# Kernel tuning notes

Measured on AMD Instinct MI355X. Metric: run time of the kernel, lower is better.

The kernel has to match this reference:

```python
import math
import jax, jax.numpy as jnp
import numpy as np

WH, WW = 8, 8
NUM_HEADS = 4
EMBED_DIMS = 128
N_TOK = WH * WW

# --- static relative position index (N, N) ---
_coords = np.stack(np.meshgrid(np.arange(WH), np.arange(WW), indexing='ij')).reshape(2, -1)
_rel = (_coords[:, :, None] - _coords[:, None, :]).transpose(1, 2, 0).copy()
_rel[..., 0] += WH - 1
_rel[..., 1] += WW - 1
_rel[..., 0] *= 2 * WW - 1
REL_INDEX = _rel.sum(-1)  # (N, N) ints in [0, (2Wh-1)(2Ww-1))

# --- static log-spaced relative coords table ((2Wh-1)*(2Ww-1), 2) ---
_ch = np.arange(-(WH - 1), WH, dtype=np.float32)
_cw = np.arange(-(WW - 1), WW, dtype=np.float32)
_tab = np.stack(np.meshgrid(_ch, _cw, indexing='ij')).reshape(2, -1).T.copy()
_tab[:, 0] /= WH - 1
_tab[:, 1] /= WW - 1
_tab *= 8
COORDS_TABLE = np.sign(_tab) * np.log2(np.abs(_tab) + 1.0) / math.log2(8)  # (225, 2)


def setup_inputs() -> dict:
    key = jax.random.key(0)
    ks = jax.random.split(key, 8)
    B_ = 8192
    C = EMBED_DIMS
    H = NUM_HEADS
    return {
        'x': jax.random.normal(ks[0], (B_, N_TOK, C), dtype=jnp.float32),
        'mask': jnp.zeros((256, N_TOK, N_TOK), dtype=jnp.float32),
        'qkv_w': jax.random.normal(ks[1], (3 * C, C), dtype=jnp.float32) * 0.02,
        'q_bias': jnp.zeros((C,), dtype=jnp.float32),
        'v_bias': jnp.zeros((C,), dtype=jnp.float32),
        'logit_scale': jnp.full((H, 1, 1), math.log(10.0), dtype=jnp.float32),
        'cpb_w1': jax.random.normal(ks[2], (512, 2), dtype=jnp.float32) * 0.02,
        'cpb_b1': jnp.zeros((512,), dtype=jnp.float32),
        'cpb_w2': jax.random.normal(ks[3], (H, 512), dtype=jnp.float32) * 0.02,
        'proj_w': jax.random.normal(ks[4], (C, C), dtype=jnp.float32) * 0.02,
        'proj_b': jnp.zeros((C,), dtype=jnp.float32),
    }


def reference(x, mask, qkv_w, q_bias, v_bias, logit_scale, cpb_w1, cpb_b1, cpb_w2, proj_w, proj_b):
    B_, N, C = x.shape
    H = NUM_HEADS
    D = C // H
    # qkv with q/v bias only (k bias is zero)
    qkv_b = jnp.concatenate([q_bias, jnp.zeros_like(v_bias), v_bias])
    qkv = x @ qkv_w.T + qkv_b                           # (B_, N, 3C)
    qkv = qkv.reshape(B_, N, 3, H, D).transpose(2, 0, 3, 1, 4)
    q, k, v = qkv[0], qkv[1], qkv[2]                    # (B_, H, N, D)
    # cosine attention
    qn = q / jnp.clip(jnp.linalg.norm(q, axis=-1, keepdims=True), 1e-12)
    kn = k / jnp.clip(jnp.linalg.norm(k, axis=-1, keepdims=True), 1e-12)
    attn = jnp.einsum('bhnd,bhmd->bhnm', qn, kn)
    scale = jnp.exp(jnp.minimum(logit_scale, math.log(1.0 / 0.01)))  # (H,1,1)
    attn = attn * scale
    # log-CPB relative position bias
    table = jnp.asarray(COORDS_TABLE, dtype=x.dtype)     # (225, 2)
    hdn = jax.nn.relu(table @ cpb_w1.T + cpb_b1)         # (225, 512)
    bias_table = hdn @ cpb_w2.T                          # (225, H)
    rel_idx = jnp.asarray(REL_INDEX.reshape(-1))
    bias = bias_table[rel_idx].reshape(N, N, H).transpose(2, 0, 1)
    bias = 16.0 * jax.nn.sigmoid(bias)                   # (H, N, N)
    attn = attn + bias[None]
    # shifted-window mask
    nW = mask.shape[0]
    attn = attn.reshape(B_ // nW, nW, H, N, N) + mask[None, :, None]
    attn = jax.nn.softmax(attn.reshape(B_, H, N, N), axis=-1)
    out = jnp.einsum('bhnm,bhmd->bhnd', attn, v)
    out = out.transpose(0, 2, 1, 3).reshape(B_, N, C)
    return out @ proj_w.T + proj_b
```

## Files before the change

### kernel.cpp

```cpp
#include <hip/hip_runtime.h>

typedef __attribute__((ext_vector_type(8))) __bf16 bf16x8;
typedef __attribute__((ext_vector_type(4))) float floatx4;

#define WS_BIAS  131072
#define WS_SCALE 196608
#define WS_TBL   196640
#define WS_ETAB  262144

static __device__ __forceinline__ unsigned short f2bf_u(float f) {
  union { __bf16 b; unsigned short u; } cv; cv.b = (__bf16)f; return cv.u;
}
static __device__ __forceinline__ unsigned pkbf(float lo, float hi) {
  union { __bf16 b[2]; unsigned u; } cv; cv.b[0] = (__bf16)lo; cv.b[1] = (__bf16)hi; return cv.u;
}
static __device__ __forceinline__ float bfu_lo(unsigned u) { return __uint_as_float(u << 16); }
static __device__ __forceinline__ float bfu_hi(unsigned u) { return __uint_as_float(u & 0xffff0000u); }

__global__ void k_prep_weights(const float* __restrict__ qkv_w,
                               const float* __restrict__ proj_w,
                               const float* __restrict__ logit_scale,
                               unsigned short* __restrict__ wsQ,
                               float* __restrict__ wsScale)
{
  int t = blockIdx.x * 256 + threadIdx.x;
  int i4 = t * 4;
  float4 v;
  if (i4 < 49152) v = *reinterpret_cast<const float4*>(qkv_w + i4);
  else            v = *reinterpret_cast<const float4*>(proj_w + (i4 - 49152));
  ushort4 pk;
  pk.x = f2bf_u(v.x); pk.y = f2bf_u(v.y); pk.z = f2bf_u(v.z); pk.w = f2bf_u(v.w);
  *reinterpret_cast<ushort4*>(wsQ + i4) = pk;
  if (t < 4) wsScale[t] = expf(fminf(logit_scale[t], 4.6051702f));
}

__global__ void k_cpb_table(const float* __restrict__ w1, const float* __restrict__ b1,
                            const float* __restrict__ w2, float* __restrict__ tbl)
{
  __shared__ float red[256][4];
  int t = blockIdx.x;
  int i = t / 15, j = t % 15;
  float c0 = 8.f * (float)(i - 7) / 7.f;
  float c1 = 8.f * (float)(j - 7) / 7.f;
  c0 = copysignf(log2f(fabsf(c0) + 1.f) / 3.f, c0);
  c1 = copysignf(log2f(fabsf(c1) + 1.f) / 3.f, c1);
  float a0 = 0.f, a1 = 0.f, a2 = 0.f, a3 = 0.f;
  for (int k = threadIdx.x; k < 512; k += 256) {
    float hd = fmaxf(c0 * w1[2*k] + c1 * w1[2*k+1] + b1[k], 0.f);
    a0 += hd * w2[k]; a1 += hd * w2[512+k]; a2 += hd * w2[1024+k]; a3 += hd * w2[1536+k];
  }
  red[threadIdx.x][0]=a0; red[threadIdx.x][1]=a1; red[threadIdx.x][2]=a2; red[threadIdx.x][3]=a3;
  __syncthreads();
  for (int s = 128; s > 0; s >>= 1) {
    if (threadIdx.x < (unsigned)s) {
      red[threadIdx.x][0] += red[threadIdx.x+s][0];
      red[threadIdx.x][1] += red[threadIdx.x+s][1];
      red[threadIdx.x][2] += red[threadIdx.x+s][2];
      red[threadIdx.x][3] += red[threadIdx.x+s][3];
    }
    __syncthreads();
  }
  if (threadIdx.x < 4) tbl[t*4 + threadIdx.x] = red[0][threadIdx.x];
}

__global__ void k_cpb_bias(const float* __restrict__ tbl, float* __restrict__ biasT)
{
  int idx = blockIdx.x * 256 + threadIdx.x;
  int hh = idx >> 12, n = (idx >> 6) & 63, m = idx & 63;
  int rel = ((n >> 3) - (m >> 3) + 7) * 15 + ((n & 7) - (m & 7) + 7);
  float bv = tbl[rel * 4 + hh];
  biasT[idx] = 16.f / (1.f + expf(-bv));
}

__global__ void k_exp_table(const float* __restrict__ biasT, const float* __restrict__ mask,
                            unsigned short* __restrict__ E)
{
  int idx4 = (blockIdx.x * 256 + threadIdx.x) * 4;
  int wm  = idx4 >> 14;
  int rem = idx4 & 16383;
  int hh  = rem >> 12;
  int nm  = rem & 4095;
  float4 mv = *reinterpret_cast<const float4*>(mask + (wm << 12) + nm);
  float4 bv = *reinterpret_cast<const float4*>(biasT + (hh << 12) + nm);
  ushort4 o;
  o.x = f2bf_u(expf(bv.x + mv.x));
  o.y = f2bf_u(expf(bv.y + mv.y));
  o.z = f2bf_u(expf(bv.z + mv.z));
  o.w = f2bf_u(expf(bv.w + mv.w));
  *reinterpret_cast<ushort4*>(E + idx4) = o;
}

__global__ __launch_bounds__(256, 2) void k_wmsa(
    const float* __restrict__ x,
    const unsigned short* __restrict__ wqkv, const unsigned short* __restrict__ wproj,
    const float* __restrict__ q_bias, const float* __restrict__ v_bias,
    const unsigned short* __restrict__ Etab, const float* __restrict__ scale4,
    const float* __restrict__ proj_b, float* __restrict__ out)
{
  __shared__ char s_x[64 * 256];
  __shared__ char s_qk[4][8192];
  __shared__ char s_vT[4][4096];

  const int blk  = blockIdx.x;
  const int tid  = threadIdx.x;
  const int lane = tid & 63;
  const int h    = tid >> 6;
  const int l15  = lane & 15;
  const int lh   = lane >> 4;
  const int swq  = ((l15 ^ (l15 >> 2)) & 3) << 4;
  const int swp  = (l15 & 7) << 4;
  const floatx4 zf4 = {0.f, 0.f, 0.f, 0.f};

  bf16x8 wvf[4][2], wff[4][4];
  #pragma unroll
  for (int kk = 0; kk < 4; ++kk) {
    #pragma unroll
    for (int ft = 0; ft < 2; ++ft)
      wvf[kk][ft] = *reinterpret_cast<const bf16x8*>(
          wqkv + (size_t)(256 + h * 32 + ft * 16 + l15) * 128 + kk * 32 + lh * 8);
    #pragma unroll
    for (int ff = 0; ff < 4; ++ff) {
      int fb = (ff < 2) ? (h * 32 + ff * 16) : (128 + h * 32 + (ff - 2) * 16);
      wff[kk][ff] = *reinterpret_cast<const bf16x8*>(
          wqkv + (size_t)(fb + l15) * 128 + kk * 32 + lh * 8);
    }
  }
  floatx4 qb0 = *reinterpret_cast<const floatx4*>(q_bias + h * 32 + lh * 4);
  floatx4 qb1 = *reinterpret_cast<const floatx4*>(q_bias + h * 32 + 16 + lh * 4);
  const float vb0 = v_bias[h * 32 + l15], vb1 = v_bias[h * 32 + 16 + l15];
  const float sc  = scale4[h] * 1.44269504f;
  const unsigned short* Eh = Etab + ((size_t)((blk & 255) * 4 + h)) * 4096;

  #pragma unroll
  for (int wi = 0; wi < 2; ++wi) {
    const size_t b = (size_t)blk + (size_t)wi * 4096;

    if (wi) __syncthreads();

    {
      const float* xb = x + b * 8192;
      int r = tid >> 2;
      #pragma unroll
      for (int cc = 0; cc < 8; ++cc) {
        int c = (tid & 3) + cc * 4;
        float4 v = reinterpret_cast<const float4*>(xb)[r * 32 + c];
        uint2 w; w.x = pkbf(v.x, v.y); w.y = pkbf(v.z, v.w);
        *reinterpret_cast<uint2*>(s_x + r * 256 + ((c * 8) ^ ((r & 7) << 4))) = w;
      }
    }
    __syncthreads();

    floatx4 vacc[4][2];
    floatx4 qk[4][4];
    #pragma unroll
    for (int mt = 0; mt < 4; ++mt) { vacc[mt][0] = zf4; vacc[mt][1] = zf4; }
    #pragma unroll
    for (int ff = 0; ff < 4; ++ff)
      #pragma unroll
      for (int tt = 0; tt < 4; ++tt) qk[ff][tt] = zf4;

    #pragma unroll
    for (int kk = 0; kk < 4; ++kk) {
      bf16x8 xf[4];
      #pragma unroll
      for (int tt = 0; tt < 4; ++tt) {
        int row = tt * 16 + l15;
        xf[tt] = *reinterpret_cast<const bf16x8*>(
            s_x + row * 256 + (((kk * 32 + lh * 8) * 2) ^ ((row & 7) << 4)));
      }
      #pragma unroll
      for (int ft = 0; ft < 2; ++ft)
        #pragma unroll
        for (int mt = 0; mt < 4; ++mt)
          vacc[mt][ft] = __builtin_amdgcn_mfma_f32_16x16x32_bf16(xf[mt], wvf[kk][ft], vacc[mt][ft], 0, 0, 0);
      #pragma unroll
      for (int ff = 0; ff < 4; ++ff)
        #pragma unroll
        for (int tt = 0; tt < 4; ++tt)
          qk[ff][tt] = __builtin_amdgcn_mfma_f32_16x16x32_bf16(wff[kk][ff], xf[tt], qk[ff][tt], 0, 0, 0);
    }

    {
      char* sv = s_vT[h];
      #pragma unroll
      for (int mt = 0; mt < 4; ++mt) {
        #pragma unroll
        for (int ft = 0; ft < 2; ++ft) {
          float vb = ft ? vb1 : vb0;
          int d = ft * 16 + l15;
          uint2 w;
          w.x = pkbf(vacc[mt][ft][0] + vb, vacc[mt][ft][1] + vb);
          w.y = pkbf(vacc[mt][ft][2] + vb, vacc[mt][ft][3] + vb);
          *reinterpret_cast<uint2*>(sv + d * 128 + (((mt * 16 + lh * 4) * 2) ^ swp)) = w;
        }
      }
    }

    #pragma unroll
    for (int tt = 0; tt < 4; ++tt)
      #pragma unroll
      for (int r = 0; r < 4; ++r) { qk[0][tt][r] += qb0[r]; qk[1][tt][r] += qb1[r]; }
    #pragma unroll
    for (int tt = 0; tt < 4; ++tt) {
      float sq = 0.f, sk = 0.f;
      #pragma unroll
      for (int r = 0; r < 4; ++r) {
        sq += qk[0][tt][r] * qk[0][tt][r] + qk[1][tt][r] * qk[1][tt][r];
        sk += qk[2][tt][r] * qk[2][tt][r] + qk[3][tt][r] * qk[3][tt][r];
      }
      sq += __shfl_xor(sq, 16); sq += __shfl_xor(sq, 32);
      sk += __shfl_xor(sk, 16); sk += __shfl_xor(sk, 32);
      float rq = sc  / fmaxf(sqrtf(sq), 1e-12f);
      float rk = 1.f / fmaxf(sqrtf(sk), 1e-12f);
      #pragma unroll
      for (int r = 0; r < 4; ++r) {
        qk[0][tt][r] *= rq; qk[1][tt][r] *= rq;
        qk[2][tt][r] *= rk; qk[3][tt][r] *= rk;
      }
    }

    uint2 e[4][4];
    #pragma unroll
    for (int tn = 0; tn < 4; ++tn)
      #pragma unroll
      for (int tm = 0; tm < 4; ++tm)
        e[tn][tm] = *reinterpret_cast<const uint2*>(
            Eh + (tn * 16 + l15) * 64 + tm * 16 + lh * 4);

    {
      char* sq = s_qk[h];
      #pragma unroll
      for (int tt = 0; tt < 4; ++tt) {
        int row = 16 * tt + l15;
        #pragma unroll
        for (int ff = 0; ff < 2; ++ff) {
          uint2 wq_, wk_;
          wq_.x = pkbf(qk[ff][tt][0],     qk[ff][tt][1]);
          wq_.y = pkbf(qk[ff][tt][2],     qk[ff][tt][3]);
          wk_.x = pkbf(qk[2 + ff][tt][0], qk[2 + ff][tt][1]);
          wk_.y = pkbf(qk[2 + ff][tt][2], qk[2 + ff][tt][3]);
          int colb = (ff * 32 + lh * 8) ^ swq;
          *reinterpret_cast<uint2*>(sq + row * 64 + colb)        = wq_;
          *reinterpret_cast<uint2*>(sq + 4096 + row * 64 + colb) = wk_;
        }
      }
    }

    floatx4 rs;
    {
      const char* sq = s_qk[h];
      bf16x8 qf[4], kf[4];
      #pragma unroll
      for (int tt = 0; tt < 4; ++tt) {
        int row = 16 * tt + l15;
        qf[tt] = *reinterpret_cast<const bf16x8*>(sq + row * 64 + ((lh * 16) ^ swq));
        kf[tt] = *reinterpret_cast<const bf16x8*>(sq + 4096 + row * 64 + ((lh * 16) ^ swq));
      }
      char* sp = s_qk[h];

      #pragma unroll
      for (int tn = 0; tn < 4; ++tn) {
        floatx4 sacc[4];
        #pragma unroll
        for (int tm = 0; tm < 4; ++tm)
          sacc[tm] = __builtin_amdgcn_mfma_f32_16x16x32_bf16(kf[tm], qf[tn], zf4, 0, 0, 0);
        float sum = 0.f;
        uint2 pw[4];
        #pragma unroll
        for (int tm = 0; tm < 4; ++tm) {
          uint2 eu = e[tn][tm];
          float e0 = exp2f(sacc[tm][0]) * bfu_lo(eu.x);
          float e1 = exp2f(sacc[tm][1]) * bfu_hi(eu.x);
          float e2 = exp2f(sacc[tm][2]) * bfu_lo(eu.y);
          float e3 = exp2f(sacc[tm][3]) * bfu_hi(eu.y);
          sum += (e0 + e1) + (e2 + e3);
          pw[tm].x = pkbf(e0, e1); pw[tm].y = pkbf(e2, e3);
        }
        sum += __shfl_xor(sum, 16); sum += __shfl_xor(sum, 32);
        rs[tn] = 1.f / sum;
        int prow = 16 * tn + l15;
        #pragma unroll
        for (int tm = 0; tm < 4; ++tm)
          *reinterpret_cast<uint2*>(sp + prow * 128 + ((tm * 32 + lh * 8) ^ swp)) = pw[tm];
      }
    }

    floatx4 oacc[2][4];
    #pragma unroll
    for (int dt = 0; dt < 2; ++dt)
      #pragma unroll
      for (int nt = 0; nt < 4; ++nt) oacc[dt][nt] = zf4;
    {
      const char* sv = s_vT[h];
      const char* sp = s_qk[h];
      #pragma unroll
      for (int kk = 0; kk < 2; ++kk) {
        bf16x8 vf[2];
        #pragma unroll
        for (int dt = 0; dt < 2; ++dt)
          vf[dt] = *reinterpret_cast<const bf16x8*>(
              sv + (dt * 16 + l15) * 128 + ((kk * 64 + lh * 16) ^ swp));
        #pragma unroll
        for (int nt = 0; nt < 4; ++nt) {
          bf16x8 pf = *reinterpret_cast<const bf16x8*>(
              sp + (nt * 16 + l15) * 128 + ((kk * 64 + lh * 16) ^ swp));
          #pragma unroll
          for (int dt = 0; dt < 2; ++dt)
            oacc[dt][nt] = __builtin_amdgcn_mfma_f32_16x16x32_bf16(vf[dt], pf, oacc[dt][nt], 0, 0, 0);
        }
      }
    }
    __syncthreads();

    #pragma unroll
    for (int dt = 0; dt < 2; ++dt) {
      #pragma unroll
      for (int nt = 0; nt < 4; ++nt) {
        int n = nt * 16 + l15;
        uint2 w;
        w.x = pkbf(oacc[dt][nt][0] * rs[nt], oacc[dt][nt][1] * rs[nt]);
        w.y = pkbf(oacc[dt][nt][2] * rs[nt], oacc[dt][nt][3] * rs[nt]);
        *reinterpret_cast<uint2*>(
            s_x + n * 256 + (((h * 32 + dt * 16 + lh * 4) * 2) ^ ((n & 7) << 4))) = w;
      }
    }
    __syncthreads();

    floatx4 pacc[4][2];
    #pragma unroll
    for (int mt = 0; mt < 4; ++mt) { pacc[mt][0] = zf4; pacc[mt][1] = zf4; }
    #pragma unroll
    for (int kk = 0; kk < 4; ++kk) {
      bf16x8 of[4];
      #pragma unroll
      for (int mt = 0; mt < 4; ++mt) {
        int row = mt * 16 + l15;
        of[mt] = *reinterpret_cast<const bf16x8*>(
            s_x + row * 256 + (((kk * 32 + lh * 8) * 2) ^ ((row & 7) << 4)));
      }
      #pragma unroll
      for (int ft = 0; ft < 2; ++ft) {
        bf16x8 wpf = *reinterpret_cast<const bf16x8*>(
            wproj + (size_t)(h * 32 + ft * 16 + l15) * 128 + kk * 32 + lh * 8);
        #pragma unroll
        for (int mt = 0; mt < 4; ++mt)
          pacc[mt][ft] = __builtin_amdgcn_mfma_f32_16x16x32_bf16(of[mt], wpf, pacc[mt][ft], 0, 0, 0);
      }
    }
    {
      float pb0 = proj_b[h * 32 + l15], pb1 = proj_b[h * 32 + 16 + l15];
      float* ob = out + b * 8192;
      #pragma unroll
      for (int mt = 0; mt < 4; ++mt)
        #pragma unroll
        for (int r = 0; r < 4; ++r) {
          int n = mt * 16 + lh * 4 + r;
          ob[n * 128 + h * 32 + l15]      = pacc[mt][0][r] + pb0;
          ob[n * 128 + h * 32 + 16 + l15] = pacc[mt][1][r] + pb1;
        }
    }
  }
}

extern "C" void kernel_launch(void* const* d_in, const int* in_sizes, int n_in,
                              void* d_out, int out_size, void* d_ws, size_t ws_size,
                              hipStream_t stream)
{
  const float* x    = (const float*)d_in[0];
  const float* mask = (const float*)d_in[1];
  const float* qkvw = (const float*)d_in[2];
  const float* qb   = (const float*)d_in[3];
  const float* vb   = (const float*)d_in[4];
  const float* ls   = (const float*)d_in[5];
  const float* w1   = (const float*)d_in[6];
  const float* b1   = (const float*)d_in[7];
  const float* w2   = (const float*)d_in[8];
  const float* pw   = (const float*)d_in[9];
  const float* pb   = (const float*)d_in[10];
  float* out = (float*)d_out;
  char* ws = (char*)d_ws;

  unsigned short* wsQ = (unsigned short*)ws;
  float* wsBias  = (float*)(ws + WS_BIAS);
  float* wsScale = (float*)(ws + WS_SCALE);
  float* wsTbl   = (float*)(ws + WS_TBL);
  unsigned short* wsE = (unsigned short*)(ws + WS_ETAB);

  hipLaunchKernelGGL(k_prep_weights, dim3(64), dim3(256), 0, stream, qkvw, pw, ls, wsQ, wsScale);
  hipLaunchKernelGGL(k_cpb_table, dim3(225), dim3(256), 0, stream, w1, b1, w2, wsTbl);
  hipLaunchKernelGGL(k_cpb_bias, dim3(64), dim3(256), 0, stream, wsTbl, wsBias);
  hipLaunchKernelGGL(k_exp_table, dim3(4096), dim3(256), 0, stream, wsBias, mask, wsE);
  hipLaunchKernelGGL(k_wmsa, dim3(4096), dim3(256), 0, stream, x,
                     wsQ, wsQ + 49152, qb, vb, wsE, wsScale, pb, out);
}
```

Baseline: 289.5 us.

## Split QKV projection into V and QK phases to cut live registers

```diff
diff --git a/kernel.cpp b/kernel.cpp
--- a/kernel.cpp
+++ b/kernel.cpp
@@ -111,29 +111,32 @@
   const int swp  = (l15 & 7) << 4;
   const floatx4 zf4 = {0.f, 0.f, 0.f, 0.f};
 
-  bf16x8 wvf[4][2], wff[4][4];
-  #pragma unroll
-  for (int kk = 0; kk < 4; ++kk) {
-    #pragma unroll
-    for (int ft = 0; ft < 2; ++ft)
-      wvf[kk][ft] = *reinterpret_cast<const bf16x8*>(
-          wqkv + (size_t)(256 + h * 32 + ft * 16 + l15) * 128 + kk * 32 + lh * 8);
-    #pragma unroll
-    for (int ff = 0; ff < 4; ++ff) {
-      int fb = (ff < 2) ? (h * 32 + ff * 16) : (128 + h * 32 + (ff - 2) * 16);
-      wff[kk][ff] = *reinterpret_cast<const bf16x8*>(
-          wqkv + (size_t)(fb + l15) * 128 + kk * 32 + lh * 8);
-    }
-  }
   floatx4 qb0 = *reinterpret_cast<const floatx4*>(q_bias + h * 32 + lh * 4);
   floatx4 qb1 = *reinterpret_cast<const floatx4*>(q_bias + h * 32 + 16 + lh * 4);
   const float vb0 = v_bias[h * 32 + l15], vb1 = v_bias[h * 32 + 16 + l15];
   const float sc  = scale4[h] * 1.44269504f;
+  const float pb0 = proj_b[h * 32 + l15], pb1 = proj_b[h * 32 + 16 + l15];
   const unsigned short* Eh = Etab + ((size_t)((blk & 255) * 4 + h)) * 4096;
+
+  uint2 e[4][4];
+  #pragma unroll
+  for (int tn = 0; tn < 4; ++tn)
+    #pragma unroll
+    for (int tm = 0; tm < 4; ++tm)
+      e[tn][tm] = *reinterpret_cast<const uint2*>(
+          Eh + (tn * 16 + l15) * 64 + tm * 16 + lh * 4);
 
   #pragma unroll
   for (int wi = 0; wi < 2; ++wi) {
     const size_t b = (size_t)blk + (size_t)wi * 4096;
+
+    bf16x8 wv[4][2];
+    #pragma unroll
+    for (int kk = 0; kk < 4; ++kk)
+      #pragma unroll
+      for (int ft = 0; ft < 2; ++ft)
+        wv[kk][ft] = *reinterpret_cast<const bf16x8*>(
+            wqkv + (size_t)(256 + h * 32 + ft * 16 + l15) * 128 + kk * 32 + lh * 8);
 
     if (wi) __syncthreads();
 
@@ -150,37 +153,25 @@
     }
     __syncthreads();
 
-    floatx4 vacc[4][2];
-    floatx4 qk[4][4];
-    #pragma unroll
-    for (int mt = 0; mt < 4; ++mt) { vacc[mt][0] = zf4; vacc[mt][1] = zf4; }
-    #pragma unroll
-    for (int ff = 0; ff < 4; ++ff)
-      #pragma unroll
-      for (int tt = 0; tt < 4; ++tt) qk[ff][tt] = zf4;
-
-    #pragma unroll
-    for (int kk = 0; kk < 4; ++kk) {
-      bf16x8 xf[4];
-      #pragma unroll
-      for (int tt = 0; tt < 4; ++tt) {
-        int row = tt * 16 + l15;
-        xf[tt] = *reinterpret_cast<const bf16x8*>(
-            s_x + row * 256 + (((kk * 32 + lh * 8) * 2) ^ ((row & 7) << 4)));
-      }
-      #pragma unroll
-      for (int ft = 0; ft < 2; ++ft)
-        #pragma unroll
-        for (int mt = 0; mt < 4; ++mt)
-          vacc[mt][ft] = __builtin_amdgcn_mfma_f32_16x16x32_bf16(xf[mt], wvf[kk][ft], vacc[mt][ft], 0, 0, 0);
-      #pragma unroll
-      for (int ff = 0; ff < 4; ++ff)
-        #pragma unroll
-        for (int tt = 0; tt < 4; ++tt)
-          qk[ff][tt] = __builtin_amdgcn_mfma_f32_16x16x32_bf16(wff[kk][ff], xf[tt], qk[ff][tt], 0, 0, 0);
-    }
-
-    {
+    {
+      floatx4 vacc[4][2];
+      #pragma unroll
+      for (int mt = 0; mt < 4; ++mt) { vacc[mt][0] = zf4; vacc[mt][1] = zf4; }
+      #pragma unroll
+      for (int kk = 0; kk < 4; ++kk) {
+        bf16x8 xf[4];
+        #pragma unroll
+        for (int tt = 0; tt < 4; ++tt) {
+          int row = tt * 16 + l15;
+          xf[tt] = *reinterpret_cast<const bf16x8*>(
+              s_x + row * 256 + (((kk * 32 + lh * 8) * 2) ^ ((row & 7) << 4)));
+        }
+        #pragma unroll
+        for (int ft = 0; ft < 2; ++ft)
+          #pragma unroll
+          for (int mt = 0; mt < 4; ++mt)
+            vacc[mt][ft] = __builtin_amdgcn_mfma_f32_16x16x32_bf16(xf[mt], wv[kk][ft], vacc[mt][ft], 0, 0, 0);
+      }
       char* sv = s_vT[h];
       #pragma unroll
       for (int mt = 0; mt < 4; ++mt) {
@@ -196,38 +187,59 @@
       }
     }
 
-    #pragma unroll
-    for (int tt = 0; tt < 4; ++tt)
-      #pragma unroll
-      for (int r = 0; r < 4; ++r) { qk[0][tt][r] += qb0[r]; qk[1][tt][r] += qb1[r]; }
-    #pragma unroll
-    for (int tt = 0; tt < 4; ++tt) {
-      float sq = 0.f, sk = 0.f;
-      #pragma unroll
-      for (int r = 0; r < 4; ++r) {
-        sq += qk[0][tt][r] * qk[0][tt][r] + qk[1][tt][r] * qk[1][tt][r];
-        sk += qk[2][tt][r] * qk[2][tt][r] + qk[3][tt][r] * qk[3][tt][r];
-      }
-      sq += __shfl_xor(sq, 16); sq += __shfl_xor(sq, 32);
-      sk += __shfl_xor(sk, 16); sk += __shfl_xor(sk, 32);
-      float rq = sc  / fmaxf(sqrtf(sq), 1e-12f);
-      float rk = 1.f / fmaxf(sqrtf(sk), 1e-12f);
-      #pragma unroll
-      for (int r = 0; r < 4; ++r) {
-        qk[0][tt][r] *= rq; qk[1][tt][r] *= rq;
-        qk[2][tt][r] *= rk; qk[3][tt][r] *= rk;
-      }
-    }
-
-    uint2 e[4][4];
-    #pragma unroll
-    for (int tn = 0; tn < 4; ++tn)
-      #pragma unroll
-      for (int tm = 0; tm < 4; ++tm)
-        e[tn][tm] = *reinterpret_cast<const uint2*>(
-            Eh + (tn * 16 + l15) * 64 + tm * 16 + lh * 4);
-
-    {
+    bf16x8 qf[4], kf[4];
+    {
+      bf16x8 wqk[4][4];
+      #pragma unroll
+      for (int kk = 0; kk < 4; ++kk)
+        #pragma unroll
+        for (int ff = 0; ff < 4; ++ff) {
+          int fb = (ff < 2) ? (h * 32 + ff * 16) : (128 + h * 32 + (ff - 2) * 16);
+          wqk[kk][ff] = *reinterpret_cast<const bf16x8*>(
+              wqkv + (size_t)(fb + l15) * 128 + kk * 32 + lh * 8);
+        }
+      floatx4 qacc[2][4], kacc[2][4];
+      #pragma unroll
+      for (int ff = 0; ff < 2; ++ff)
+        #pragma unroll
+        for (int tt = 0; tt < 4; ++tt) { qacc[ff][tt] = zf4; kacc[ff][tt] = zf4; }
+      #pragma unroll
+      for (int kk = 0; kk < 4; ++kk) {
+        bf16x8 xf[4];
+        #pragma unroll
+        for (int tt = 0; tt < 4; ++tt) {
+          int row = tt * 16 + l15;
+          xf[tt] = *reinterpret_cast<const bf16x8*>(
+              s_x + row * 256 + (((kk * 32 + lh * 8) * 2) ^ ((row & 7) << 4)));
+        }
+        #pragma unroll
+        for (int ff = 0; ff < 2; ++ff)
+          #pragma unroll
+          for (int tt = 0; tt < 4; ++tt) {
+            qacc[ff][tt] = __builtin_amdgcn_mfma_f32_16x16x32_bf16(wqk[kk][ff],     xf[tt], qacc[ff][tt], 0, 0, 0);
+            kacc[ff][tt] = __builtin_amdgcn_mfma_f32_16x16x32_bf16(wqk[kk][2 + ff], xf[tt], kacc[ff][tt], 0, 0, 0);
+          }
+      }
+      #pragma unroll
+      for (int tt = 0; tt < 4; ++tt) {
+        #pragma unroll
+        for (int r = 0; r < 4; ++r) { qacc[0][tt][r] += qb0[r]; qacc[1][tt][r] += qb1[r]; }
+        float sq = 0.f, sk = 0.f;
+        #pragma unroll
+        for (int r = 0; r < 4; ++r) {
+          sq += qacc[0][tt][r] * qacc[0][tt][r] + qacc[1][tt][r] * qacc[1][tt][r];
+          sk += kacc[0][tt][r] * kacc[0][tt][r] + kacc[1][tt][r] * kacc[1][tt][r];
+        }
+        sq += __shfl_xor(sq, 16); sq += __shfl_xor(sq, 32);
+        sk += __shfl_xor(sk, 16); sk += __shfl_xor(sk, 32);
+        float rq = sc / fmaxf(sqrtf(sq), 1e-12f);
+        float rk = 1.f / fmaxf(sqrtf(sk), 1e-12f);
+        #pragma unroll
+        for (int r = 0; r < 4; ++r) {
+          qacc[0][tt][r] *= rq; qacc[1][tt][r] *= rq;
+          kacc[0][tt][r] *= rk; kacc[1][tt][r] *= rk;
+        }
+      }
       char* sq = s_qk[h];
       #pragma unroll
       for (int tt = 0; tt < 4; ++tt) {
@@ -235,29 +247,26 @@
         #pragma unroll
         for (int ff = 0; ff < 2; ++ff) {
           uint2 wq_, wk_;
-          wq_.x = pkbf(qk[ff][tt][0],     qk[ff][tt][1]);
-          wq_.y = pkbf(qk[ff][tt][2],     qk[ff][tt][3]);
-          wk_.x = pkbf(qk[2 + ff][tt][0], qk[2 + ff][tt][1]);
-          wk_.y = pkbf(qk[2 + ff][tt][2], qk[2 + ff][tt][3]);
+          wq_.x = pkbf(qacc[ff][tt][0], qacc[ff][tt][1]);
+          wq_.y = pkbf(qacc[ff][tt][2], qacc[ff][tt][3]);
+          wk_.x = pkbf(kacc[ff][tt][0], kacc[ff][tt][1]);
+          wk_.y = pkbf(kacc[ff][tt][2], kacc[ff][tt][3]);
           int colb = (ff * 32 + lh * 8) ^ swq;
           *reinterpret_cast<uint2*>(sq + row * 64 + colb)        = wq_;
           *reinterpret_cast<uint2*>(sq + 4096 + row * 64 + colb) = wk_;
         }
       }
-    }
-
-    floatx4 rs;
-    {
-      const char* sq = s_qk[h];
-      bf16x8 qf[4], kf[4];
       #pragma unroll
       for (int tt = 0; tt < 4; ++tt) {
         int row = 16 * tt + l15;
         qf[tt] = *reinterpret_cast<const bf16x8*>(sq + row * 64 + ((lh * 16) ^ swq));
         kf[tt] = *reinterpret_cast<const bf16x8*>(sq + 4096 + row * 64 + ((lh * 16) ^ swq));
       }
+    }
+
+    floatx4 rs;
+    {
       char* sp = s_qk[h];
-
       #pragma unroll
       for (int tn = 0; tn < 4; ++tn) {
         floatx4 sacc[4];
@@ -326,29 +335,32 @@
     }
     __syncthreads();
 
-    floatx4 pacc[4][2];
-    #pragma unroll
-    for (int mt = 0; mt < 4; ++mt) { pacc[mt][0] = zf4; pacc[mt][1] = zf4; }
-    #pragma unroll
-    for (int kk = 0; kk < 4; ++kk) {
-      bf16x8 of[4];
-      #pragma unroll
-      for (int mt = 0; mt < 4; ++mt) {
-        int row = mt * 16 + l15;
-        of[mt] = *reinterpret_cast<const bf16x8*>(
-            s_x + row * 256 + (((kk * 32 + lh * 8) * 2) ^ ((row & 7) << 4)));
-      }
-      #pragma unroll
-      for (int ft = 0; ft < 2; ++ft) {
-        bf16x8 wpf = *reinterpret_cast<const bf16x8*>(
-            wproj + (size_t)(h * 32 + ft * 16 + l15) * 128 + kk * 32 + lh * 8);
-        #pragma unroll
-        for (int mt = 0; mt < 4; ++mt)
-          pacc[mt][ft] = __builtin_amdgcn_mfma_f32_16x16x32_bf16(of[mt], wpf, pacc[mt][ft], 0, 0, 0);
-      }
-    }
-    {
-      float pb0 = proj_b[h * 32 + l15], pb1 = proj_b[h * 32 + 16 + l15];
+    {
+      bf16x8 wp[4][2];
+      #pragma unroll
+      for (int kk = 0; kk < 4; ++kk)
+        #pragma unroll
+        for (int ft = 0; ft < 2; ++ft)
+          wp[kk][ft] = *reinterpret_cast<const bf16x8*>(
+              wproj + (size_t)(h * 32 + ft * 16 + l15) * 128 + kk * 32 + lh * 8);
+      floatx4 pacc[4][2];
+      #pragma unroll
+      for (int mt = 0; mt < 4; ++mt) { pacc[mt][0] = zf4; pacc[mt][1] = zf4; }
+      #pragma unroll
+      for (int kk = 0; kk < 4; ++kk) {
+        bf16x8 of[4];
+        #pragma unroll
+        for (int mt = 0; mt < 4; ++mt) {
+          int row = mt * 16 + l15;
+          of[mt] = *reinterpret_cast<const bf16x8*>(
+              s_x + row * 256 + (((kk * 32 + lh * 8) * 2) ^ ((row & 7) << 4)));
+        }
+        #pragma unroll
+        for (int ft = 0; ft < 2; ++ft)
+          #pragma unroll
+          for (int mt = 0; mt < 4; ++mt)
+            pacc[mt][ft] = __builtin_amdgcn_mfma_f32_16x16x32_bf16(of[mt], wp[kk][ft], pacc[mt][ft], 0, 0, 0);
+      }
       float* ob = out + b * 8192;
       #pragma unroll
       for (int mt = 0; mt < 4; ++mt)
```

New measurement: 296.7 us. 2.5% more time.
